# Kernel tuning notes

Hardware: AMD Instinct MI355X
Metric: run time of the kernel (lower is better)

Reference implementation:

```python
import jax, jax.numpy as jnp
import numpy as np

B, L, F_DIM, H = 4, 384, 640, 128
K_COULOMB = 332.0
DIELECTRIC = 80.0
BN_EPS = 1e-5

# amino-acid charge table, index order 'ACDEFGHIKLMNPQRSTVWY'
_AA = 'ACDEFGHIKLMNPQRSTVWY'
_CHG = {'D': -1.0, 'E': -1.0, 'K': 1.0, 'R': 1.0, 'H': 0.1}
_TABLE = np.zeros((20, 3), dtype=np.float32)
for _i, _aa in enumerate(_AA):
    c = _CHG.get(_aa, 0.0)
    _TABLE[_i, 0 if c > 0 else (1 if c < 0 else 2)] = 1.0
CHG_TABLE = jnp.asarray(_TABLE)


def _conv1d(x, w, b, pad):
    # x: [N, Cin, L], w: [Cout, Cin, K]
    y = jax.lax.conv_general_dilated(x, w, (1,), [(pad, pad)],
                                     dimension_numbers=('NCH', 'OIH', 'NCH'))
    return y + b[None, :, None]


def setup_inputs() -> dict:
    key = jax.random.key(0)
    ks = jax.random.split(key, 32)
    s = 0.05

    def rn(k, shape):
        return (jax.random.normal(k, shape) * s).astype(jnp.float32)

    inp = {
        'features': jax.random.normal(ks[0], (B, L, F_DIM), dtype=jnp.float32),
        'seq_ids': jax.random.randint(ks[1], (B, L), 0, 20, dtype=jnp.int32),
        'structures': (jax.random.normal(ks[2], (B, L, 3)) * 10.0).astype(jnp.float32),
        # charge predictor: Linear(F,H) -> ReLU -> BN(H) -> Linear(H,H//2) -> ReLU -> Linear(H//2,3) -> Softmax
        'W1': rn(ks[3], (F_DIM, H)), 'b1': jnp.zeros((H,), jnp.float32),
        'gamma': jnp.ones((H,), jnp.float32), 'beta': jnp.zeros((H,), jnp.float32),
        'rmean': jnp.zeros((H,), jnp.float32), 'rvar': jnp.ones((H,), jnp.float32),
        'W2': rn(ks[4], (H, H // 2)), 'b2': jnp.zeros((H // 2,), jnp.float32),
        'W3': rn(ks[5], (H // 2, 3)), 'b3': jnp.zeros((3,), jnp.float32),
        # salt bridge detector: Linear(2F+1,H) -> ReLU -> Linear(H,64) -> ReLU -> Linear(64,1) -> Sigmoid
        'sW1': rn(ks[6], (2 * F_DIM + 1, H)), 'sb1': jnp.zeros((H,), jnp.float32),
        'sW2': rn(ks[7], (H, 64)), 'sb2': jnp.zeros((64,), jnp.float32),
        'sW3': rn(ks[8], (64, 1)), 'sb3': jnp.zeros((1,), jnp.float32),
        # potential calculator convs (OIH layout)
        'c1w': rn(ks[9], (16, 1, 5)), 'c1b': jnp.zeros((16,), jnp.float32),
        'c2w': rn(ks[10], (8, 16, 3)), 'c2b': jnp.zeros((8,), jnp.float32),
        'c3w': rn(ks[11], (1, 8, 3)), 'c3b': jnp.zeros((1,), jnp.float32),
    }
    return inp


def reference(features, seq_ids, structures,
              W1, b1, gamma, beta, rmean, rvar, W2, b2, W3, b3,
              sW1, sb1, sW2, sb2, sW3, sb3,
              c1w, c1b, c2w, c2b, c3w, c3b):
    b_, l_, f_ = features.shape

    # true charges from sequence (one-hot pos/neg/neutral)
    true_charges = CHG_TABLE[seq_ids]                               # [B,L,3]

    # --- charge predictor (BatchNorm in eval mode: running stats) ---
    x = features.reshape(-1, f_)
    h = jax.nn.relu(x @ W1 + b1)
    h = gamma * (h - rmean) / jnp.sqrt(rvar + BN_EPS) + beta
    h = jax.nn.relu(h @ W2 + b2)
    pc = jax.nn.softmax(h @ W3 + b3, axis=-1).reshape(b_, l_, 3)    # [B,L,3]

    net_charge = pc[:, :, 0:1] - pc[:, :, 1:2]                      # [B,L,1]

    # --- electrostatic potential: 1D conv stack on [B,1,L] ---
    p = net_charge.transpose(0, 2, 1)                               # [B,1,L]
    p = jax.nn.relu(_conv1d(p, c1w, c1b, 2))
    p = jax.nn.relu(_conv1d(p, c2w, c2b, 1))
    p = _conv1d(p, c3w, c3b, 1)
    potential = p.transpose(0, 2, 1)                                # [B,L,1]

    # --- pairwise distances ---
    diff = structures[:, :, None, :] - structures[:, None, :, :]    # [B,L,L,3]
    D = jnp.sqrt(jnp.sum(diff * diff, axis=-1) + 1e-12)             # [B,L,L]

    # --- salt bridges: vectorized edge-MLP over all (pos i, neg j) pairs ---
    pos = pc[:, :, 0] > pc[:, :, 2]                                 # [B,L]
    neg = pc[:, :, 1] > pc[:, :, 2]                                 # [B,L]
    a, bb, d = sW1[:f_], sW1[f_:2 * f_], sW1[2 * f_]                # split cat([fi,fj,dist]) @ sW1
    fi = features @ a                                               # [B,L,H]
    fj = features @ bb                                              # [B,L,H]
    hid = jax.nn.relu(fi[:, :, None, :] + fj[:, None, :, :] + D[..., None] * d + sb1)  # [B,L,L,H]
    hid2 = jax.nn.relu(hid @ sW2 + sb2)                             # [B,L,L,64]
    prob = jax.nn.sigmoid((hid2 @ sW3 + sb3)[..., 0])               # [B,L,L]
    q = pos[:, :, None] & neg[:, None, :] & (D < 4.0) & (prob > 0.5)
    salt_bridge_masks = (q | q.transpose(0, 2, 1)).astype(jnp.float32)  # [B,L,L]

    # --- Coulomb energy with distance-dependent dielectric ---
    # dielectric = eps * D / 4 -> e_ij = k * q_i q_j / (eps/4 * D^2)
    qc = pc[:, :, 0] - pc[:, :, 1]                                  # [B,L]
    valid = (D < 15.0) & (D > 0.0)
    triu = jnp.triu(jnp.ones((l_, l_), bool), k=1)[None]
    D_safe = jnp.where(valid, D, 1.0)
    e_ij = K_COULOMB * qc[:, :, None] * qc[:, None, :] / ((DIELECTRIC / 4.0) * D_safe * D_safe)
    energy = jnp.sum(jnp.where(valid & triu, e_ij, 0.0), axis=(1, 2))  # [B]

    return (pc, true_charges, net_charge, potential, salt_bridge_masks, energy)
```

## Files before the change

### kernel.cpp

```cpp
#include <hip/hip_runtime.h>

#define LSEQ 384
#define NROWS 1536
#define FDIM 640
#define HDIM 128
#define PART 196608

#define WS_FIP (4*PART)
#define WS_FJP (8*PART)
#define WS_QC  (14*PART)
#define WS_FLAG (WS_QC + NROWS)

#define OUT_PC    0
#define OUT_TC    4608
#define OUT_NET   9216
#define OUT_POT   10752
#define OUT_MASK  12288
#define OUT_EN    602112

typedef float f4 __attribute__((ext_vector_type(4)));

__device__ __forceinline__ void gl16(const float* g, float* l) {
    __builtin_amdgcn_global_load_lds((const __attribute__((address_space(1))) float*)g,
                                     (__attribute__((address_space(3))) float*)l, 16, 0, 0);
}

__global__ __launch_bounds__(256) void kA(const float* __restrict__ X,
                                          const float* __restrict__ W1,
                                          const float* __restrict__ sW1,
                                          const float* __restrict__ b1,
                                          const float* __restrict__ gam,
                                          const float* __restrict__ bet,
                                          const float* __restrict__ rmean,
                                          const float* __restrict__ rvar,
                                          const float* __restrict__ W2,
                                          const float* __restrict__ b2,
                                          const float* __restrict__ W3,
                                          const float* __restrict__ b3,
                                          const int* __restrict__ seq,
                                          float* __restrict__ ws,
                                          float* __restrict__ out) {
    __shared__ __align__(16) float lds[18944];

    const int t  = threadIdx.x;
    const int bx = blockIdx.x;
    const int by = blockIdx.y;
    const int lane = t & 63;

    if (by == 0 && bx == 0 && t < 4) out[OUT_EN + t] = 0.0f;

    if (by >= 2) {
        const int by2 = by - 2;
        const int mat = by2 >> 2;
        const int kz  = by2 & 3;
        const int m0  = bx * 32;
        const float* W = sW1 + mat * FDIM * HDIM;
        float* O = ws + (mat == 0 ? WS_FIP : WS_FJP) + kz * PART;
        const int k0 = kz * 160;

        float* As = lds;
        float* Bs = lds + 2304;

        const int wv = t >> 6;
        const int rg = t >> 5, cg = t & 31;
        const int ar = t >> 3, ac4 = (t & 7) * 4;

        auto stage_B = [&](int buf, int kk) {
            const float* src = W + (long)kk * HDIM;
            float* dst = Bs + buf * 4096;
#pragma unroll
            for (int i = 0; i < 4; i++) {
                const int c = wv * 4 + i;
                gl16(src + c * 256 + lane * 4, dst + c * 256);
            }
        };

        f4 acc[4];
        acc[0] = acc[1] = acc[2] = acc[3] = (f4){0.f, 0.f, 0.f, 0.f};

        stage_B(0, k0);
        {
            f4 av = *(const f4*)&X[(long)(m0 + ar) * FDIM + k0 + ac4];
            As[(ac4 + 0) * 36 + ar] = av[0];
            As[(ac4 + 1) * 36 + ar] = av[1];
            As[(ac4 + 2) * 36 + ar] = av[2];
            As[(ac4 + 3) * 36 + ar] = av[3];
        }
        __syncthreads();

        for (int kt = 0; kt < 5; kt++) {
            const int buf = kt & 1;
            f4 av;
            if (kt < 4) {
                const int kk = k0 + (kt + 1) * 32;
                stage_B(buf ^ 1, kk);
                av = *(const f4*)&X[(long)(m0 + ar) * FDIM + kk + ac4];
            }
            const float* Ab = As + buf * 1152;
            const float* Bb = Bs + buf * 4096;
#pragma unroll
            for (int k = 0; k < 32; k++) {
                f4 a = *(const f4*)&Ab[k * 36 + rg * 4];
                f4 b = *(const f4*)&Bb[k * 128 + cg * 4];
                acc[0] += a[0] * b;
                acc[1] += a[1] * b;
                acc[2] += a[2] * b;
                acc[3] += a[3] * b;
            }
            if (kt < 4) {
                float* Aw = As + (buf ^ 1) * 1152;
                Aw[(ac4 + 0) * 36 + ar] = av[0];
                Aw[(ac4 + 1) * 36 + ar] = av[1];
                Aw[(ac4 + 2) * 36 + ar] = av[2];
                Aw[(ac4 + 3) * 36 + ar] = av[3];
            }
            __syncthreads();
        }

#pragma unroll
        for (int r = 0; r < 4; r++)
            *(f4*)&O[(long)(m0 + rg * 4 + r) * HDIM + cg * 4] = acc[r];
        return;
    }

    const int hb = by * 48 + bx;
    const int m0 = hb * 16;
    const int g  = t >> 7;
    const int tg = t & 127;
    const int wvg = tg >> 6;
    const int rg = tg >> 5;
    const int cg = tg & 31;
    const int ar = tg >> 3, ac4 = (tg & 7) * 4;
    const int k0g = g * 320;

    float* As = lds + g * 9472;
    float* Bs = lds + g * 9472 + 1280;

    auto stage_Bh = [&](int buf, int kk) {
        const float* src = W1 + (long)kk * HDIM;
        float* dst = Bs + buf * 4096;
#pragma unroll
        for (int i = 0; i < 8; i++) {
            const int c = wvg * 8 + i;
            gl16(src + c * 256 + lane * 4, dst + c * 256);
        }
    };

    f4 acc[4];
    acc[0] = acc[1] = acc[2] = acc[3] = (f4){0.f, 0.f, 0.f, 0.f};

    stage_Bh(0, k0g);
    {
        f4 av = *(const f4*)&X[(long)(m0 + ar) * FDIM + k0g + ac4];
        As[(ac4 + 0) * 20 + ar] = av[0];
        As[(ac4 + 1) * 20 + ar] = av[1];
        As[(ac4 + 2) * 20 + ar] = av[2];
        As[(ac4 + 3) * 20 + ar] = av[3];
    }
    __syncthreads();

    for (int kt = 0; kt < 10; kt++) {
        const int buf = kt & 1;
        f4 av;
        if (kt < 9) {
            const int kk = k0g + (kt + 1) * 32;
            stage_Bh(buf ^ 1, kk);
            av = *(const f4*)&X[(long)(m0 + ar) * FDIM + kk + ac4];
        }
        const float* Ab = As + buf * 640;
        const float* Bb = Bs + buf * 4096;
#pragma unroll
        for (int k = 0; k < 32; k++) {
            f4 a = *(const f4*)&Ab[k * 20 + rg * 4];
            f4 b = *(const f4*)&Bb[k * 128 + cg * 4];
            acc[0] += a[0] * b;
            acc[1] += a[1] * b;
            acc[2] += a[2] * b;
            acc[3] += a[3] * b;
        }
        if (kt < 9) {
            float* Aw = As + (buf ^ 1) * 640;
            Aw[(ac4 + 0) * 20 + ar] = av[0];
            Aw[(ac4 + 1) * 20 + ar] = av[1];
            Aw[(ac4 + 2) * 20 + ar] = av[2];
            Aw[(ac4 + 3) * 20 + ar] = av[3];
        }
        __syncthreads();
    }

    float* hs = lds;
#pragma unroll
    for (int r = 0; r < 4; r++)
        *(f4*)&hs[g * 2048 + (rg * 4 + r) * 128 + cg * 4] = acc[r];
    __syncthreads();

    if (t >= 128) return;
    const int wv01 = t >> 6;

    float h0[8], h1[8];
#pragma unroll
    for (int rr = 0; rr < 8; rr++) {
        const int rl = wv01 * 8 + rr;
        float a0 = hs[rl * 128 + lane]      + hs[2048 + rl * 128 + lane];
        float a1 = hs[rl * 128 + 64 + lane] + hs[2048 + rl * 128 + 64 + lane];
        a0 = fmaxf(a0 + b1[lane], 0.0f);
        a1 = fmaxf(a1 + b1[64 + lane], 0.0f);
        h0[rr] = gam[lane]      * (a0 - rmean[lane])      / sqrtf(rvar[lane] + 1e-5f)      + bet[lane];
        h1[rr] = gam[64 + lane] * (a1 - rmean[64 + lane]) / sqrtf(rvar[64 + lane] + 1e-5f) + bet[64 + lane];
    }

    const float b2v = b2[lane];
    float a2[8];
#pragma unroll
    for (int rr = 0; rr < 8; rr++) a2[rr] = b2v;
#pragma unroll 4
    for (int cc = 0; cc < 64; cc++) {
        const float wv0 = W2[cc * 64 + lane];
        const float wv1 = W2[(cc + 64) * 64 + lane];
#pragma unroll
        for (int rr = 0; rr < 8; rr++) {
            float hv0 = __uint_as_float(__builtin_amdgcn_readlane(__float_as_uint(h0[rr]), cc));
            float hv1 = __uint_as_float(__builtin_amdgcn_readlane(__float_as_uint(h1[rr]), cc));
            a2[rr] = fmaf(hv0, wv0, a2[rr]);
            a2[rr] = fmaf(hv1, wv1, a2[rr]);
        }
    }

    const float w30 = W3[lane * 3 + 0], w31 = W3[lane * 3 + 1], w32 = W3[lane * 3 + 2];
#pragma unroll
    for (int rr = 0; rr < 8; rr++) {
        float h2 = fmaxf(a2[rr], 0.0f);
        float x0 = h2 * w30, x1 = h2 * w31, x2 = h2 * w32;
#pragma unroll
        for (int o = 32; o > 0; o >>= 1) {
            x0 += __shfl_xor(x0, o, 64);
            x1 += __shfl_xor(x1, o, 64);
            x2 += __shfl_xor(x2, o, 64);
        }
        if (lane == 0) {
            const int row = m0 + wv01 * 8 + rr;
            float l0 = x0 + b3[0], l1 = x1 + b3[1], l2 = x2 + b3[2];
            float m = fmaxf(l0, fmaxf(l1, l2));
            float e0 = expf(l0 - m), e1 = expf(l1 - m), e2 = expf(l2 - m);
            float s = e0 + e1 + e2;
            float pc0 = e0 / s, pc1 = e1 / s, pc2 = e2 / s;
            out[OUT_PC + row * 3 + 0] = pc0;
            out[OUT_PC + row * 3 + 1] = pc1;
            out[OUT_PC + row * 3 + 2] = pc2;
            float net = pc0 - pc1;
            out[OUT_NET + row] = net;
            ws[WS_QC + row] = net;
            ((int*)(ws + WS_FLAG))[row] = (pc0 > pc2 ? 1 : 0) | (pc1 > pc2 ? 2 : 0);
            int sid = seq[row];
            float c0 = (sid == 6 || sid == 8 || sid == 14) ? 1.0f : 0.0f;
            float c1 = (sid == 2 || sid == 3) ? 1.0f : 0.0f;
            out[OUT_TC + row * 3 + 0] = c0;
            out[OUT_TC + row * 3 + 1] = c1;
            out[OUT_TC + row * 3 + 2] = (c0 == 0.0f && c1 == 0.0f) ? 1.0f : 0.0f;
        }
    }
}

__device__ __forceinline__ float mlp_eval(const float* __restrict__ fip, const float* __restrict__ fjp,
                                          int gi, int gj, float D,
                                          float dv0, float dv1, float sb0, float sb1v,
                                          float b2v, float w3l, const float* w2s, int lane) {
    const long bi0 = (long)gi * 128 + lane;
    const long bj0 = (long)gj * 128 + lane;
    float fi0 = ((fip[bi0] + fip[PART + bi0]) + fip[2 * PART + bi0]) + fip[3 * PART + bi0];
    float fi1 = ((fip[bi0 + 64] + fip[PART + bi0 + 64]) + fip[2 * PART + bi0 + 64]) + fip[3 * PART + bi0 + 64];
    float fj0 = ((fjp[bj0] + fjp[PART + bj0]) + fjp[2 * PART + bj0]) + fjp[3 * PART + bj0];
    float fj1 = ((fjp[bj0 + 64] + fjp[PART + bj0 + 64]) + fjp[2 * PART + bj0 + 64]) + fjp[3 * PART + bj0 + 64];
    float h0 = fmaxf(fi0 + fj0 + D * dv0 + sb0, 0.0f);
    float h1 = fmaxf(fi1 + fj1 + D * dv1 + sb1v, 0.0f);
    float a0 = 0.0f, a1 = 0.0f;
#pragma unroll
    for (int cc = 0; cc < 64; cc++) {
        float hv0 = __uint_as_float(__builtin_amdgcn_readlane(__float_as_uint(h0), cc));
        float hv1 = __uint_as_float(__builtin_amdgcn_readlane(__float_as_uint(h1), cc));
        a0 = fmaf(hv0, w2s[cc * 64 + lane], a0);
        a1 = fmaf(hv1, w2s[(cc + 64) * 64 + lane], a1);
    }
    float x = fmaxf(a0 + a1 + b2v, 0.0f) * w3l;
#pragma unroll
    for (int o = 32; o > 0; o >>= 1) x += __shfl_xor(x, o, 64);
    return x;
}

__global__ __launch_bounds__(256) void k2(const float* __restrict__ S,
                                          const float* __restrict__ ws,
                                          const float* __restrict__ sW1,
                                          const float* __restrict__ sb1,
                                          const float* __restrict__ sW2,
                                          const float* __restrict__ sb2,
                                          const float* __restrict__ sW3,
                                          const float* __restrict__ sb3,
                                          const float* __restrict__ c1w, const float* __restrict__ c1b,
                                          const float* __restrict__ c2w, const float* __restrict__ c2b,
                                          const float* __restrict__ c3w, const float* __restrict__ c3b,
                                          float* __restrict__ out) {
    __shared__ char smem[40960];
    const int t = threadIdx.x;
    const int bi = blockIdx.x;

    if (bi < 4) {
        float* p0 = (float*)smem;
        float* p1 = p0 + 388;
        float* p2 = p1 + 16 * 386;
        const int b = bi;
        for (int j = t; j < LSEQ; j += 256) p0[j + 2] = out[OUT_NET + b * LSEQ + j];
        if (t < 2) { p0[t] = 0.0f; p0[LSEQ + 2 + t] = 0.0f; }
        if (t < 16) { p1[t * 386] = 0.0f; p1[t * 386 + 385] = 0.0f; }
        if (t < 8)  { p2[t * 386] = 0.0f; p2[t * 386 + 385] = 0.0f; }
        __syncthreads();
        for (int pos = t; pos < LSEQ; pos += 256) {
#pragma unroll
            for (int o = 0; o < 16; o++) {
                float acc = c1b[o];
#pragma unroll
                for (int k = 0; k < 5; k++) acc = fmaf(p0[pos + k], c1w[o * 5 + k], acc);
                p1[o * 386 + pos + 1] = fmaxf(acc, 0.0f);
            }
        }
        __syncthreads();
        for (int pos = t; pos < LSEQ; pos += 256) {
#pragma unroll
            for (int o = 0; o < 8; o++) {
                float acc = c2b[o];
                for (int i = 0; i < 16; i++)
#pragma unroll
                    for (int k = 0; k < 3; k++)
                        acc = fmaf(p1[i * 386 + pos + k], c2w[(o * 16 + i) * 3 + k], acc);
                p2[o * 386 + pos + 1] = fmaxf(acc, 0.0f);
            }
        }
        __syncthreads();
        for (int pos = t; pos < LSEQ; pos += 256) {
            float acc = c3b[0];
            for (int i = 0; i < 8; i++)
#pragma unroll
                for (int k = 0; k < 3; k++)
                    acc = fmaf(p2[i * 386 + pos + k], c3w[i * 3 + k], acc);
            out[OUT_POT + b * LSEQ + pos] = acc;
        }
        return;
    }

    float* sx = (float*)smem;
    float* sy = sx + 384;
    float* sz = sy + 384;
    float* sq = sz + 384;
    unsigned int* clist = (unsigned int*)(sx + 1536);
    unsigned char* sf = (unsigned char*)(smem + 7680);
    float* red = (float*)(smem + 8064);
    int* cntL = (int*)(smem + 8080);
    int* w2flag = (int*)(smem + 8084);
    float* w2s = (float*)(smem + 8192);

    const float* qc = ws + WS_QC;
    const int* flags = (const int*)(ws + WS_FLAG);
    const float* fip = ws + WS_FIP;
    const float* fjp = ws + WS_FJP;

    const int rowblk = bi - 4;
    const int b = rowblk / 96;
    const int i0 = (rowblk % 96) * 4;

    for (int j = t; j < LSEQ; j += 256) {
        int g = b * LSEQ + j;
        sx[j] = S[g * 3 + 0];
        sy[j] = S[g * 3 + 1];
        sz[j] = S[g * 3 + 2];
        sq[j] = qc[g];
        sf[j] = (unsigned char)flags[g];
    }
    if (t == 0) *w2flag = 0;
    __syncthreads();

    const int lane = t & 63, w = t >> 6;
    const float* dvec = sW1 + 1280 * 128;
    const float dv0 = dvec[lane], dv1 = dvec[lane + 64];
    const float sb0 = sb1[lane], sb1v = sb1[lane + 64];
    const float w3l = sW3[lane];
    const float b2v = sb2[lane];
    const float b3v = sb3[0];

    float esum = 0.0f;

    for (int r = 0; r < 4; r++) {
        const int i = i0 + r;
        const int grow = b * LSEQ + i;
        if (t == 0) *cntL = 0;
        __syncthreads();

        const float six = sx[i], siy = sy[i], siz = sz[i], qi = sq[i];
        const int fli = sf[i];
        const bool posi = (fli & 1) != 0, negi = (fli & 2) != 0;
        float* mrow = out + OUT_MASK + (long)grow * LSEQ;

        for (int j = t; j < LSEQ; j += 256) {
            float dx = __fsub_rn(six, sx[j]);
            float dy = __fsub_rn(siy, sy[j]);
            float dz = __fsub_rn(siz, sz[j]);
            float d2 = __fadd_rn(__fadd_rn(__fmul_rn(dx, dx), __fmul_rn(dy, dy)), __fmul_rn(dz, dz));
            d2 = __fadd_rn(d2, 1e-12f);
            float D = __fsqrt_rn(d2);
            mrow[j] = 0.0f;
            if (j > i && D < 15.0f && D > 0.0f) {
                float num = __fmul_rn(__fmul_rn(332.0f, qi), sq[j]);
                float den = __fmul_rn(__fmul_rn(20.0f, D), D);
                esum += __fdiv_rn(num, den);
            }
            int flj = sf[j];
            bool near = (D < 4.0f);
            bool need1 = near && posi && ((flj & 2) != 0);
            bool need2 = near && negi && ((flj & 1) != 0);
            if (need1 || need2) {
                int p = atomicAdd(cntL, 1);
                clist[p] = (unsigned int)j | (need1 ? 512u : 0u) | (need2 ? 1024u : 0u);
            }
        }
        __syncthreads();

        int nc = *cntL;
        if (nc > 0) {
            if (!*w2flag) {
                for (int idx = t; idx < 2048; idx += 256)
                    ((float4*)w2s)[idx] = ((const float4*)sW2)[idx];
                __syncthreads();
                if (t == 0) *w2flag = 1;
            }
            for (int c = w; c < nc; c += 4) {
                unsigned int e = clist[c];
                int j = (int)(e & 511u);
                bool need1 = (e & 512u) != 0, need2 = (e & 1024u) != 0;
                float dx = __fsub_rn(six, sx[j]);
                float dy = __fsub_rn(siy, sy[j]);
                float dz = __fsub_rn(siz, sz[j]);
                float d2 = __fadd_rn(__fadd_rn(__fmul_rn(dx, dx), __fmul_rn(dy, dy)), __fmul_rn(dz, dz));
                d2 = __fadd_rn(d2, 1e-12f);
                float D = __fsqrt_rn(d2);
                int gi = grow, gj = b * LSEQ + j;
                bool hit = false;
                if (need1) {
                    float x = mlp_eval(fip, fjp, gi, gj, D, dv0, dv1, sb0, sb1v, b2v, w3l, w2s, lane);
                    hit = (x + b3v) > 0.0f;
                }
                if (!hit && need2) {
                    float x = mlp_eval(fip, fjp, gj, gi, D, dv0, dv1, sb0, sb1v, b2v, w3l, w2s, lane);
                    hit = (x + b3v) > 0.0f;
                }
                if (hit && lane == 0) mrow[j] = 1.0f;
            }
        }
        __syncthreads();
    }

#pragma unroll
    for (int o = 32; o > 0; o >>= 1) esum += __shfl_xor(esum, o, 64);
    if (lane == 0) red[w] = esum;
    __syncthreads();
    if (t == 0) {
        float s = red[0] + red[1] + red[2] + red[3];
        atomicAdd(&out[OUT_EN + b], s);
    }
}

extern "C" void kernel_launch(void* const* d_in, const int* in_sizes, int n_in,
                              void* d_out, int out_size, void* d_ws, size_t ws_size,
                              hipStream_t stream) {
    const float* X     = (const float*)d_in[0];
    const int*   seq   = (const int*)d_in[1];
    const float* S     = (const float*)d_in[2];
    const float* W1    = (const float*)d_in[3];
    const float* b1    = (const float*)d_in[4];
    const float* gam   = (const float*)d_in[5];
    const float* bet   = (const float*)d_in[6];
    const float* rmean = (const float*)d_in[7];
    const float* rvar  = (const float*)d_in[8];
    const float* W2    = (const float*)d_in[9];
    const float* b2    = (const float*)d_in[10];
    const float* W3    = (const float*)d_in[11];
    const float* b3    = (const float*)d_in[12];
    const float* sW1   = (const float*)d_in[13];
    const float* sb1   = (const float*)d_in[14];
    const float* sW2   = (const float*)d_in[15];
    const float* sb2   = (const float*)d_in[16];
    const float* sW3   = (const float*)d_in[17];
    const float* sb3   = (const float*)d_in[18];
    const float* c1w   = (const float*)d_in[19];
    const float* c1b   = (const float*)d_in[20];
    const float* c2w   = (const float*)d_in[21];
    const float* c2b   = (const float*)d_in[22];
    const float* c3w   = (const float*)d_in[23];
    const float* c3b   = (const float*)d_in[24];

    float* out = (float*)d_out;
    float* ws  = (float*)d_ws;

    hipLaunchKernelGGL(kA, dim3(48, 10), dim3(256), 0, stream,
                       X, W1, sW1, b1, gam, bet, rmean, rvar, W2, b2, W3, b3, seq, ws, out);
    hipLaunchKernelGGL(k2, dim3(388), dim3(256), 0, stream,
                       S, ws, sW1, sb1, sW2, sb2, sW3, sb3,
                       c1w, c1b, c2w, c2b, c3w, c3b, out);
}
```

Baseline: 159.0 us.

## Unify kA GEMM paths with 32-row tiles and full-K W1 blocks

The charge-predictor GEMM path moves from 96 blocks, each with two 128-thread groups splitting K over 16-row tiles, to 48 blocks that each run 32 rows over the full K=640 with the same 32x128 tile loop as the salt-bridge partial GEMMs. The grid shrinks from 48x10 to 48x9 and LDS per block drops, and the cross-group reduction through shared memory goes away. The trade is that these 48 blocks now run 20 K-iterations against 5 for the other blocks, which may lengthen the critical path of kA. It also halves the parallelism given to the W1 path and the MLP tail.

```diff
diff --git a/kernel.cpp b/kernel.cpp
--- a/kernel.cpp
+++ b/kernel.cpp
@@ -40,108 +40,35 @@
                                           const int* __restrict__ seq,
                                           float* __restrict__ ws,
                                           float* __restrict__ out) {
-    __shared__ __align__(16) float lds[18944];
+    __shared__ __align__(16) float lds[10496];
 
     const int t  = threadIdx.x;
     const int bx = blockIdx.x;
     const int by = blockIdx.y;
-    const int lane = t & 63;
+    const int lane = t & 63, wv = t >> 6;
+    const int rg = t >> 5, cg = t & 31;
+    const int ar = t >> 3, ac4 = (t & 7) * 4;
+    const int m0 = bx * 32;
 
     if (by == 0 && bx == 0 && t < 4) out[OUT_EN + t] = 0.0f;
 
-    if (by >= 2) {
-        const int by2 = by - 2;
-        const int mat = by2 >> 2;
-        const int kz  = by2 & 3;
-        const int m0  = bx * 32;
-        const float* W = sW1 + mat * FDIM * HDIM;
-        float* O = ws + (mat == 0 ? WS_FIP : WS_FJP) + kz * PART;
-        const int k0 = kz * 160;
-
-        float* As = lds;
-        float* Bs = lds + 2304;
-
-        const int wv = t >> 6;
-        const int rg = t >> 5, cg = t & 31;
-        const int ar = t >> 3, ac4 = (t & 7) * 4;
-
-        auto stage_B = [&](int buf, int kk) {
-            const float* src = W + (long)kk * HDIM;
-            float* dst = Bs + buf * 4096;
-#pragma unroll
-            for (int i = 0; i < 4; i++) {
-                const int c = wv * 4 + i;
-                gl16(src + c * 256 + lane * 4, dst + c * 256);
-            }
-        };
-
-        f4 acc[4];
-        acc[0] = acc[1] = acc[2] = acc[3] = (f4){0.f, 0.f, 0.f, 0.f};
-
-        stage_B(0, k0);
-        {
-            f4 av = *(const f4*)&X[(long)(m0 + ar) * FDIM + k0 + ac4];
-            As[(ac4 + 0) * 36 + ar] = av[0];
-            As[(ac4 + 1) * 36 + ar] = av[1];
-            As[(ac4 + 2) * 36 + ar] = av[2];
-            As[(ac4 + 3) * 36 + ar] = av[3];
-        }
-        __syncthreads();
-
-        for (int kt = 0; kt < 5; kt++) {
-            const int buf = kt & 1;
-            f4 av;
-            if (kt < 4) {
-                const int kk = k0 + (kt + 1) * 32;
-                stage_B(buf ^ 1, kk);
-                av = *(const f4*)&X[(long)(m0 + ar) * FDIM + kk + ac4];
-            }
-            const float* Ab = As + buf * 1152;
-            const float* Bb = Bs + buf * 4096;
-#pragma unroll
-            for (int k = 0; k < 32; k++) {
-                f4 a = *(const f4*)&Ab[k * 36 + rg * 4];
-                f4 b = *(const f4*)&Bb[k * 128 + cg * 4];
-                acc[0] += a[0] * b;
-                acc[1] += a[1] * b;
-                acc[2] += a[2] * b;
-                acc[3] += a[3] * b;
-            }
-            if (kt < 4) {
-                float* Aw = As + (buf ^ 1) * 1152;
-                Aw[(ac4 + 0) * 36 + ar] = av[0];
-                Aw[(ac4 + 1) * 36 + ar] = av[1];
-                Aw[(ac4 + 2) * 36 + ar] = av[2];
-                Aw[(ac4 + 3) * 36 + ar] = av[3];
-            }
-            __syncthreads();
-        }
-
-#pragma unroll
-        for (int r = 0; r < 4; r++)
-            *(f4*)&O[(long)(m0 + rg * 4 + r) * HDIM + cg * 4] = acc[r];
-        return;
-    }
-
-    const int hb = by * 48 + bx;
-    const int m0 = hb * 16;
-    const int g  = t >> 7;
-    const int tg = t & 127;
-    const int wvg = tg >> 6;
-    const int rg = tg >> 5;
-    const int cg = tg & 31;
-    const int ar = tg >> 3, ac4 = (tg & 7) * 4;
-    const int k0g = g * 320;
-
-    float* As = lds + g * 9472;
-    float* Bs = lds + g * 9472 + 1280;
-
-    auto stage_Bh = [&](int buf, int kk) {
-        const float* src = W1 + (long)kk * HDIM;
+    float* As = lds;
+    float* Bs = lds + 2304;
+
+    const int h1path = (by == 0);
+    const int by2 = by - 1;
+    const int mat = h1path ? 0 : (by2 >> 2);
+    const int kz  = h1path ? 0 : (by2 & 3);
+    const float* W = h1path ? W1 : (sW1 + mat * FDIM * HDIM);
+    const int k0 = kz * 160;
+    const int NT = h1path ? 20 : 5;
+
+    auto stage_B = [&](int buf, int kk) {
+        const float* src = W + (long)kk * HDIM;
         float* dst = Bs + buf * 4096;
 #pragma unroll
-        for (int i = 0; i < 8; i++) {
-            const int c = wvg * 8 + i;
+        for (int i = 0; i < 4; i++) {
+            const int c = wv * 4 + i;
             gl16(src + c * 256 + lane * 4, dst + c * 256);
         }
     };
@@ -149,60 +76,65 @@
     f4 acc[4];
     acc[0] = acc[1] = acc[2] = acc[3] = (f4){0.f, 0.f, 0.f, 0.f};
 
-    stage_Bh(0, k0g);
+    stage_B(0, k0);
     {
-        f4 av = *(const f4*)&X[(long)(m0 + ar) * FDIM + k0g + ac4];
-        As[(ac4 + 0) * 20 + ar] = av[0];
-        As[(ac4 + 1) * 20 + ar] = av[1];
-        As[(ac4 + 2) * 20 + ar] = av[2];
-        As[(ac4 + 3) * 20 + ar] = av[3];
+        f4 av = *(const f4*)&X[(long)(m0 + ar) * FDIM + k0 + ac4];
+        As[(ac4 + 0) * 36 + ar] = av[0];
+        As[(ac4 + 1) * 36 + ar] = av[1];
+        As[(ac4 + 2) * 36 + ar] = av[2];
+        As[(ac4 + 3) * 36 + ar] = av[3];
     }
     __syncthreads();
 
-    for (int kt = 0; kt < 10; kt++) {
+    for (int kt = 0; kt < NT; kt++) {
         const int buf = kt & 1;
         f4 av;
-        if (kt < 9) {
-            const int kk = k0g + (kt + 1) * 32;
-            stage_Bh(buf ^ 1, kk);
+        if (kt < NT - 1) {
+            const int kk = k0 + (kt + 1) * 32;
+            stage_B(buf ^ 1, kk);
             av = *(const f4*)&X[(long)(m0 + ar) * FDIM + kk + ac4];
         }
-        const float* Ab = As + buf * 640;
+        const float* Ab = As + buf * 1152;
         const float* Bb = Bs + buf * 4096;
 #pragma unroll
         for (int k = 0; k < 32; k++) {
-            f4 a = *(const f4*)&Ab[k * 20 + rg * 4];
+            f4 a = *(const f4*)&Ab[k * 36 + rg * 4];
             f4 b = *(const f4*)&Bb[k * 128 + cg * 4];
             acc[0] += a[0] * b;
             acc[1] += a[1] * b;
             acc[2] += a[2] * b;
             acc[3] += a[3] * b;
         }
-        if (kt < 9) {
-            float* Aw = As + (buf ^ 1) * 640;
-            Aw[(ac4 + 0) * 20 + ar] = av[0];
-            Aw[(ac4 + 1) * 20 + ar] = av[1];
-            Aw[(ac4 + 2) * 20 + ar] = av[2];
-            Aw[(ac4 + 3) * 20 + ar] = av[3];
-        }
-        __syncthreads();
+        if (kt < NT - 1) {
+            float* Aw = As + (buf ^ 1) * 1152;
+            Aw[(ac4 + 0) * 36 + ar] = av[0];
+            Aw[(ac4 + 1) * 36 + ar] = av[1];
+            Aw[(ac4 + 2) * 36 + ar] = av[2];
+            Aw[(ac4 + 3) * 36 + ar] = av[3];
+        }
+        __syncthreads();
+    }
+
+    if (!h1path) {
+        float* O = ws + (mat == 0 ? WS_FIP : WS_FJP) + kz * PART;
+#pragma unroll
+        for (int r = 0; r < 4; r++)
+            *(f4*)&O[(long)(m0 + rg * 4 + r) * HDIM + cg * 4] = acc[r];
+        return;
     }
 
     float* hs = lds;
 #pragma unroll
     for (int r = 0; r < 4; r++)
-        *(f4*)&hs[g * 2048 + (rg * 4 + r) * 128 + cg * 4] = acc[r];
+        *(f4*)&hs[(rg * 4 + r) * 128 + cg * 4] = acc[r];
     __syncthreads();
 
-    if (t >= 128) return;
-    const int wv01 = t >> 6;
-
     float h0[8], h1[8];
 #pragma unroll
     for (int rr = 0; rr < 8; rr++) {
-        const int rl = wv01 * 8 + rr;
-        float a0 = hs[rl * 128 + lane]      + hs[2048 + rl * 128 + lane];
-        float a1 = hs[rl * 128 + 64 + lane] + hs[2048 + rl * 128 + 64 + lane];
+        const int rl = wv * 8 + rr;
+        float a0 = hs[rl * 128 + lane];
+        float a1 = hs[rl * 128 + 64 + lane];
         a0 = fmaxf(a0 + b1[lane], 0.0f);
         a1 = fmaxf(a1 + b1[64 + lane], 0.0f);
         h0[rr] = gam[lane]      * (a0 - rmean[lane])      / sqrtf(rvar[lane] + 1e-5f)      + bet[lane];
@@ -238,7 +170,7 @@
             x2 += __shfl_xor(x2, o, 64);
         }
         if (lane == 0) {
-            const int row = m0 + wv01 * 8 + rr;
+            const int row = m0 + wv * 8 + rr;
             float l0 = x0 + b3[0], l1 = x1 + b3[1], l2 = x2 + b3[2];
             float m = fmaxf(l0, fmaxf(l1, l2));
             float e0 = expf(l0 - m), e1 = expf(l1 - m), e2 = expf(l2 - m);
@@ -498,7 +430,7 @@
     float* out = (float*)d_out;
     float* ws  = (float*)d_ws;
 
-    hipLaunchKernelGGL(kA, dim3(48, 10), dim3(256), 0, stream,
+    hipLaunchKernelGGL(kA, dim3(48, 9), dim3(256), 0, stream,
                        X, W1, sW1, b1, gam, bet, rmean, rvar, W2, b2, W3, b3, seq, ws, out);
     hipLaunchKernelGGL(k2, dim3(388), dim3(256), 0, stream,
                        S, ws, sW1, sb1, sW2, sb2, sW3, sb3,
```

Result: slower. 170.2 us (+7.0%).
